# Optimization experiments

Hardware: AMD Instinct MI355X
Metric: run time of the kernel (lower is better)

The kernel has to match this reference:

```python
import jax, jax.numpy as jnp
import numpy as np

NUM_NODES = 50000
NUM_EDGES = 800000
NUM_FEATURES = 128
HIDDEN = 256
NUM_CLASSES = 10
NUM_GRAPHS = 64


def setup_inputs() -> dict:
    key = jax.random.key(0)
    ks = jax.random.split(key, 16)
    x = jax.random.normal(ks[0], (NUM_NODES, NUM_FEATURES), dtype=jnp.float32)
    edge_index = jax.random.randint(ks[1], (2, NUM_EDGES), 0, NUM_NODES, dtype=jnp.int64)
    batch = jnp.sort(jax.random.randint(ks[2], (NUM_NODES,), 0, NUM_GRAPHS, dtype=jnp.int64))

    def glorot(k, shape):
        fan_in, fan_out = shape[-2], shape[-1]
        s = jnp.sqrt(6.0 / (fan_in + fan_out)).astype(jnp.float32)
        return jax.random.uniform(k, shape, jnp.float32, -s, s)

    inp = {
        "x": x, "edge_index": edge_index, "batch": batch,
        # Chebyshev weights: one [in, out] matrix per hop order k
        "W1": glorot(ks[3], (3, NUM_FEATURES, HIDDEN)), "b1": jnp.zeros((HIDDEN,), jnp.float32),
        "W2": glorot(ks[4], (4, HIDDEN, HIDDEN)),       "b2": jnp.zeros((HIDDEN,), jnp.float32),
        "W3": glorot(ks[5], (5, HIDDEN, HIDDEN)),       "b3": jnp.zeros((HIDDEN,), jnp.float32),
        "fc1_w": glorot(ks[6], (HIDDEN, 512)),  "fc1_b": jnp.zeros((512,), jnp.float32),
        "fc2_w": glorot(ks[7], (512, HIDDEN)),  "fc2_b": jnp.zeros((HIDDEN,), jnp.float32),
        "fc3_w": glorot(ks[8], (HIDDEN, NUM_CLASSES)), "fc3_b": jnp.zeros((NUM_CLASSES,), jnp.float32),
    }
    return inp


def reference(x, edge_index, batch, W1, b1, W2, b2, W3, b3,
              fc1_w, fc1_b, fc2_w, fc2_b, fc3_w, fc3_b):
    N = x.shape[0]
    src, dst = edge_index[0], edge_index[1]

    # Scaled Laplacian L_hat = -D^{-1/2} A D^{-1/2} (lambda_max = 2, sym norm)
    deg = jax.ops.segment_sum(jnp.ones_like(src, dtype=x.dtype), src, num_segments=N)
    dis = jnp.where(deg > 0, jax.lax.rsqrt(jnp.maximum(deg, 1.0)), 0.0)
    w = -dis[src] * dis[dst]  # [E]

    def prop(h):  # L_hat @ h via gather-scale-scatter
        return jax.ops.segment_sum(h[src] * w[:, None], dst, num_segments=N)

    def cheb(h, Wk, b):
        K = Wk.shape[0]
        Tx0 = h
        out = Tx0 @ Wk[0]
        Tx1 = prop(h)
        out = out + Tx1 @ Wk[1]
        for k in range(2, K):
            Tx2 = 2.0 * prop(Tx1) - Tx0
            out = out + Tx2 @ Wk[k]
            Tx0, Tx1 = Tx1, Tx2
        return out + b

    h = jax.nn.relu(cheb(x, W1, b1))
    h = jax.nn.relu(cheb(h, W2, b2))
    h = jax.nn.relu(cheb(h, W3, b3))

    # global mean pool over graphs in the batch
    sums = jax.ops.segment_sum(h, batch, num_segments=NUM_GRAPHS)
    cnts = jax.ops.segment_sum(jnp.ones((N,), h.dtype), batch, num_segments=NUM_GRAPHS)
    g = sums / jnp.maximum(cnts, 1.0)[:, None]  # [G, 256]

    g = jax.nn.relu(g @ fc1_w + fc1_b)  # dropout is identity at inference
    g = jax.nn.relu(g @ fc2_w + fc2_b)
    g = g @ fc3_w + fc3_b
    return jax.nn.log_softmax(g, axis=1)
```

## Files before the change

### kernel.cpp

```cpp
#include <hip/hip_runtime.h>
#include <cstdint>
#include <cstddef>

#define NN 50000
#define NE 800000
#define FIN 128
#define HID 256
#define NCLS 10
#define NG 64
#define LDT 1280

#define NCH 13
#define NCELL (NN * NCH)
#define NSCB ((NCELL + 255) / 256)

typedef unsigned int uint;
typedef unsigned short ushort;
typedef __attribute__((ext_vector_type(8))) short short8;
typedef __attribute__((ext_vector_type(4))) float f32x4;

static inline size_t align_up(size_t v, size_t a) { return (v + a - 1) / a * a; }

__device__ __forceinline__ float bf2f(ushort u) {
    union { uint i; float f; } v; v.i = (uint)u << 16; return v.f;
}
__device__ __forceinline__ ushort f2bf(float f) {
    union { uint i; float f; } v; v.f = f;
    uint i = v.i;
    uint r = (i + 0x7fffu + ((i >> 16) & 1u)) >> 16;
    return (ushort)r;
}
__device__ __forceinline__ uint pack2(float a, float b) {
    return (uint)f2bf(a) | ((uint)f2bf(b) << 16);
}


__global__ void k_degcnt(const int* __restrict__ src, const int* __restrict__ dst,
                         int* __restrict__ ideg, int* __restrict__ cellcnt) {
    int e = blockIdx.x * 256 + threadIdx.x;
    if (e < NE) {
        int s = src[e], d = dst[e];
        atomicAdd(&ideg[s], 1);
        atomicAdd(&cellcnt[d * NCH + (s >> 12)], 1);
    }
}

__global__ void k_dis(const int* __restrict__ ideg, float* __restrict__ dis) {
    int n = blockIdx.x * 256 + threadIdx.x;
    if (n < NN) {
        int d = ideg[n];
        dis[n] = (d > 0) ? rsqrtf((float)d) : 0.0f;
    }
}

__global__ void k_scanA(const int* __restrict__ cnt, int* __restrict__ rp,
                        int* __restrict__ bsum) {
    __shared__ int s[256];
    int i = blockIdx.x * 256 + threadIdx.x;
    int v = (i < NCELL) ? cnt[i] : 0;
    s[threadIdx.x] = v;
    __syncthreads();
    for (int off = 1; off < 256; off <<= 1) {
        int t = (threadIdx.x >= (unsigned)off) ? s[threadIdx.x - off] : 0;
        __syncthreads();
        s[threadIdx.x] += t;
        __syncthreads();
    }
    if (i < NCELL) rp[i] = s[threadIdx.x] - v;
    if (threadIdx.x == 255) bsum[blockIdx.x] = s[255];
}

__global__ void k_scanB(int* __restrict__ b, int n) {
    __shared__ int s[1024];
    __shared__ int carry;
    if (threadIdx.x == 0) carry = 0;
    __syncthreads();
    for (int base = 0; base < n; base += 1024) {
        int i = base + threadIdx.x;
        int v = (i < n) ? b[i] : 0;
        s[threadIdx.x] = v;
        __syncthreads();
        for (int off = 1; off < 1024; off <<= 1) {
            int t = (threadIdx.x >= (unsigned)off) ? s[threadIdx.x - off] : 0;
            __syncthreads();
            s[threadIdx.x] += t;
            __syncthreads();
        }
        int c = carry;
        if (i < n) b[i] = c + s[threadIdx.x] - v;
        __syncthreads();
        if (threadIdx.x == 0) carry = c + s[1023];
        __syncthreads();
    }
}

__global__ void k_scanC(const int* __restrict__ bsum, int* __restrict__ rp,
                        int* __restrict__ cur, int* __restrict__ rpn) {
    int i = blockIdx.x * 256 + threadIdx.x;
    if (i < NCELL) {
        int v = rp[i] + bsum[blockIdx.x];
        rp[i] = v;
        cur[i] = v;
        if (i % NCH == 0) rpn[i / NCH] = v;
    }
    if (i == 0) rpn[NN] = NE;
}

__global__ void k_fill2(const int* __restrict__ src, const int* __restrict__ dst,
                        const float* __restrict__ dis, int* __restrict__ cur,
                        uint2* __restrict__ em) {
    int e = blockIdx.x * 256 + threadIdx.x;
    if (e < NE) {
        int s = src[e], d = dst[e];
        int pos = atomicAdd(&cur[d * NCH + (s >> 12)], 1);
        uint2 m;
        m.x = (uint)s;
        m.y = __float_as_uint(-dis[s] * dis[d]);
        em[pos] = m;
    }
}

__global__ void k_wt(const float* __restrict__ W, ushort* __restrict__ Wt, int K) {
    int i = blockIdx.x * 256 + threadIdx.x;
    if (i < K * 256) {
        int k = i >> 8, n = i & 255;
        Wt[(size_t)n * K + k] = f2bf(W[i]);
    }
}


__global__ void k_spread_x(const float* __restrict__ x, ushort* __restrict__ T) {
    int i = blockIdx.x * 256 + threadIdx.x;
    if (i < NN * 64) {
        int m = i >> 6, p = i & 63;
        const float* xp = x + (size_t)m * FIN + p * 2;
        uint* tp = (uint*)(T + (size_t)m * LDT) + p;
        *tp = pack2(xp[0], xp[1]);
    }
}

template <int FUSE, int F>
__global__ __launch_bounds__(512) void k_prop3(
    const int* __restrict__ rpn, const uint2* __restrict__ em,
    const ushort* __restrict__ h, const ushort* __restrict__ sub,
    ushort* __restrict__ out) {
    constexpr int NV = (F == 256) ? 4 : 2;
    int d = blockIdx.x * 8 + (threadIdx.x >> 6);
    int lane = threadIdx.x & 63;
    int beg = rpn[d], end = rpn[d + 1];
    float a[NV];
#pragma unroll
    for (int j = 0; j < NV; ++j) a[j] = 0.0f;

    int e = beg;
    int nfull = (end - beg) >> 3;
    if (nfull > 0) {
        uint2 mt[8];
#pragma unroll
        for (int u = 0; u < 8; ++u) mt[u] = em[e + u];
        for (int g = 0; g < nfull; ++g) {
            uint2 mtn[8];
            if (F == 256) {
                uint2 gg[8];
#pragma unroll
                for (int u = 0; u < 8; ++u)
                    gg[u] = *((const uint2*)(h + (size_t)mt[u].x * LDT) + lane);
#pragma unroll
                for (int u = 0; u < 8; ++u) {
                    int pe = e + 8 + u; if (pe > end - 1) pe = end - 1;
                    mtn[u] = em[pe];
                }
#pragma unroll
                for (int u = 0; u < 8; ++u) {
                    float wv = __uint_as_float(mt[u].y);
                    a[0] += wv * bf2f((ushort)gg[u].x);
                    a[1] += wv * bf2f((ushort)(gg[u].x >> 16));
                    a[2] += wv * bf2f((ushort)gg[u].y);
                    a[3] += wv * bf2f((ushort)(gg[u].y >> 16));
                }
            } else {
                uint gg[8];
#pragma unroll
                for (int u = 0; u < 8; ++u)
                    gg[u] = *((const uint*)(h + (size_t)mt[u].x * LDT) + lane);
#pragma unroll
                for (int u = 0; u < 8; ++u) {
                    int pe = e + 8 + u; if (pe > end - 1) pe = end - 1;
                    mtn[u] = em[pe];
                }
#pragma unroll
                for (int u = 0; u < 8; ++u) {
                    float wv = __uint_as_float(mt[u].y);
                    a[0] += wv * bf2f((ushort)gg[u]);
                    a[1] += wv * bf2f((ushort)(gg[u] >> 16));
                }
            }
#pragma unroll
            for (int u = 0; u < 8; ++u) mt[u] = mtn[u];
            e += 8;
        }
    }
    for (; e + 4 <= end; e += 4) {
        uint2 mt[4];
#pragma unroll
        for (int u = 0; u < 4; ++u) mt[u] = em[e + u];
        if (F == 256) {
            uint2 gg[4];
#pragma unroll
            for (int u = 0; u < 4; ++u)
                gg[u] = *((const uint2*)(h + (size_t)mt[u].x * LDT) + lane);
#pragma unroll
            for (int u = 0; u < 4; ++u) {
                float wv = __uint_as_float(mt[u].y);
                a[0] += wv * bf2f((ushort)gg[u].x);
                a[1] += wv * bf2f((ushort)(gg[u].x >> 16));
                a[2] += wv * bf2f((ushort)gg[u].y);
                a[3] += wv * bf2f((ushort)(gg[u].y >> 16));
            }
        } else {
            uint gg[4];
#pragma unroll
            for (int u = 0; u < 4; ++u)
                gg[u] = *((const uint*)(h + (size_t)mt[u].x * LDT) + lane);
#pragma unroll
            for (int u = 0; u < 4; ++u) {
                float wv = __uint_as_float(mt[u].y);
                a[0] += wv * bf2f((ushort)gg[u]);
                a[1] += wv * bf2f((ushort)(gg[u] >> 16));
            }
        }
    }
    for (; e < end; ++e) {
        uint2 m0 = em[e];
        float w0 = __uint_as_float(m0.y);
        if (F == 256) {
            uint2 g0 = *((const uint2*)(h + (size_t)m0.x * LDT) + lane);
            a[0] += w0 * bf2f((ushort)g0.x); a[1] += w0 * bf2f((ushort)(g0.x >> 16));
            a[2] += w0 * bf2f((ushort)g0.y); a[3] += w0 * bf2f((ushort)(g0.y >> 16));
        } else {
            uint g0 = *((const uint*)(h + (size_t)m0.x * LDT) + lane);
            a[0] += w0 * bf2f((ushort)g0); a[1] += w0 * bf2f((ushort)(g0 >> 16));
        }
    }

    if (F == 256) {
        uint2* op = (uint2*)(out + (size_t)d * LDT) + lane;
        if (FUSE) {
            uint2 sv = *((const uint2*)(sub + (size_t)d * LDT) + lane);
            uint2 r;
            r.x = pack2(2.0f * a[0] - bf2f((ushort)sv.x),
                        2.0f * a[1] - bf2f((ushort)(sv.x >> 16)));
            r.y = pack2(2.0f * a[2] - bf2f((ushort)sv.y),
                        2.0f * a[3] - bf2f((ushort)(sv.y >> 16)));
            *op = r;
        } else {
            uint2 r;
            r.x = pack2(a[0], a[1]);
            r.y = pack2(a[2], a[3]);
            *op = r;
        }
    } else {
        uint* op = (uint*)(out + (size_t)d * LDT) + lane;
        if (FUSE) {
            uint sv = *((const uint*)(sub + (size_t)d * LDT) + lane);
            *op = pack2(2.0f * a[0] - bf2f((ushort)sv),
                        2.0f * a[1] - bf2f((ushort)(sv >> 16)));
        } else {
            *op = pack2(a[0], a[1]);
        }
    }
}

template <int K>
__global__ __launch_bounds__(256) void k_mm3(
    const ushort* __restrict__ A, int lda,
    int m0, int m1, int m2, int m3, int m4,
    const ushort* __restrict__ Wt, const float* __restrict__ bias,
    ushort* __restrict__ H, int ldh, int M) {
    constexpr int NT = K / 32;
    __shared__ ushort As[3][128 * 32];
    __shared__ ushort Bs[3][128 * 32];
    int tid = threadIdx.x;
    int lane = tid & 63, w = tid >> 6;
    int wm = w >> 1, wn = w & 1;
    int rowBase = blockIdx.x * 128;
    int colBase = blockIdx.y * 128;
    int srow = lane >> 2;
    int c16 = lane & 3;

    f32x4 acc[4][4];
#pragma unroll
    for (int i = 0; i < 4; ++i)
#pragma unroll
        for (int j = 0; j < 4; ++j) acc[i][j] = (f32x4){0.f, 0.f, 0.f, 0.f};

    auto stage = [&](int t) {
        int kk = t * 32;
        int slot = kk >> 8;
        int coff = (slot == 0 ? m0 : slot == 1 ? m1 : slot == 2 ? m2
                    : slot == 3 ? m3 : m4) + (kk & 255);
        int b = t % 3;
#pragma unroll
        for (int q = 0; q < 2; ++q) {
            int seg = w * 2 + q;
            int r = seg * 16 + srow;
            int cs = c16 ^ ((r >> 1) & 3);
            int grow = rowBase + r;
            if (grow > M - 1) grow = M - 1;
            const ushort* gp = A + (size_t)grow * lda + coff + cs * 8;
            __builtin_amdgcn_global_load_lds(
                (const __attribute__((address_space(1))) void*)gp,
                (__attribute__((address_space(3))) void*)((char*)&As[b][0] + seg * 1024),
                16, 0, 0);
        }
#pragma unroll
        for (int q = 0; q < 2; ++q) {
            int seg = w * 2 + q;
            int r = seg * 16 + srow;
            int cs = c16 ^ ((r >> 1) & 3);
            const ushort* gp = Wt + (size_t)(colBase + r) * K + kk + cs * 8;
            __builtin_amdgcn_global_load_lds(
                (const __attribute__((address_space(1))) void*)gp,
                (__attribute__((address_space(3))) void*)((char*)&Bs[b][0] + seg * 1024),
                16, 0, 0);
        }
    };

    stage(0);
    stage(1);

    for (int t = 0; t < NT; ++t) {
        if (t + 1 < NT) {
            asm volatile("s_waitcnt vmcnt(4)" ::: "memory");
        } else {
            asm volatile("s_waitcnt vmcnt(0)" ::: "memory");
        }
        __builtin_amdgcn_s_barrier();
        if (t + 2 < NT) stage(t + 2);

        int b = t % 3;
        short8 af[4], bf[4];
#pragma unroll
        for (int mi = 0; mi < 4; ++mi) {
            int r = wm * 64 + mi * 16 + (lane & 15);
            int j = (lane >> 4) ^ ((r >> 1) & 3);
            af[mi] = *(const short8*)((const char*)&As[b][0] + r * 64 + j * 16);
        }
#pragma unroll
        for (int ni = 0; ni < 4; ++ni) {
            int r = wn * 64 + ni * 16 + (lane & 15);
            int j = (lane >> 4) ^ ((r >> 1) & 3);
            bf[ni] = *(const short8*)((const char*)&Bs[b][0] + r * 64 + j * 16);
        }
#pragma unroll
        for (int mi = 0; mi < 4; ++mi)
#pragma unroll
            for (int ni = 0; ni < 4; ++ni)
                acc[mi][ni] = __builtin_amdgcn_mfma_f32_16x16x32_bf16(
                    af[mi], bf[ni], acc[mi][ni], 0, 0, 0);
    }

    int lg = lane >> 4;
    float bv[4];
#pragma unroll
    for (int ni = 0; ni < 4; ++ni)
        bv[ni] = bias[colBase + wn * 64 + ni * 16 + (lane & 15)];
#pragma unroll
    for (int mi = 0; mi < 4; ++mi) {
#pragma unroll
        for (int r = 0; r < 4; ++r) {
            int row = rowBase + wm * 64 + mi * 16 + lg * 4 + r;
            if (row >= M) continue;
#pragma unroll
            for (int ni = 0; ni < 4; ++ni) {
                int colL = colBase + wn * 64 + ni * 16 + (lane & 15);
                float v = acc[mi][ni][r] + bv[ni];
                v = fmaxf(v, 0.0f);
                H[(size_t)row * ldh + colL] = f2bf(v);
            }
        }
    }
}


__global__ void k_pool(const ushort* __restrict__ h, const int* __restrict__ batch,
                       float* __restrict__ sums, float* __restrict__ cnts) {
    int f = threadIdx.x;
    int n0 = blockIdx.x * 128;
    if (n0 >= NN) return;
    int nEnd = n0 + 128 < NN ? n0 + 128 : NN;
    int cur = batch[n0];
    float acc = 0.0f, c = 0.0f;
    for (int n = n0; n < nEnd; ++n) {
        int b = batch[n];
        if (b != cur) {
            atomicAdd(&sums[cur * HID + f], acc);
            if (f == 0) atomicAdd(&cnts[cur], c);
            acc = 0.0f; c = 0.0f; cur = b;
        }
        acc += bf2f(h[(size_t)n * HID + f]);
        c += 1.0f;
    }
    atomicAdd(&sums[cur * HID + f], acc);
    if (f == 0) atomicAdd(&cnts[cur], c);
}

__global__ void k_gdiv(const float* __restrict__ sums, const float* __restrict__ cnts,
                       float* __restrict__ g) {
    int i = blockIdx.x * 256 + threadIdx.x;
    int b = i >> 8;
    g[i] = sums[i] / fmaxf(cnts[b], 1.0f);
}


template <int RELU>
__global__ void k_fc(const float* __restrict__ in, const float* __restrict__ W,
                     const float* __restrict__ bias, float* __restrict__ out,
                     int K, int Nc) {
    __shared__ float s[512];
    int gi = blockIdx.x;
    for (int i = threadIdx.x; i < K; i += blockDim.x) s[i] = in[gi * K + i];
    __syncthreads();
    int c = blockIdx.y * blockDim.x + threadIdx.x;
    if (c < Nc) {
        float acc = bias[c];
        for (int k = 0; k < K; ++k) acc += s[k] * W[k * Nc + c];
        out[gi * Nc + c] = RELU ? fmaxf(acc, 0.0f) : acc;
    }
}

__global__ void k_fc3_lsm(const float* __restrict__ in, const float* __restrict__ W,
                          const float* __restrict__ b, float* __restrict__ out) {
    __shared__ float s[HID];
    __shared__ float lg[NCLS];
    int gi = blockIdx.x;
    s[threadIdx.x] = in[gi * HID + threadIdx.x];
    __syncthreads();
    if (threadIdx.x < NCLS) {
        float acc = b[threadIdx.x];
        for (int k = 0; k < HID; ++k) acc += s[k] * W[k * NCLS + threadIdx.x];
        lg[threadIdx.x] = acc;
    }
    __syncthreads();
    if (threadIdx.x < NCLS) {
        float m = -1e30f;
        for (int c = 0; c < NCLS; ++c) m = fmaxf(m, lg[c]);
        float sum = 0.0f;
        for (int c = 0; c < NCLS; ++c) sum += expf(lg[c] - m);
        out[gi * NCLS + threadIdx.x] = lg[threadIdx.x] - m - logf(sum);
    }
}


extern "C" void kernel_launch(void* const* d_in, const int* in_sizes, int n_in,
                              void* d_out, int out_size, void* d_ws, size_t ws_size,
                              hipStream_t stream) {
    const float* x = (const float*)d_in[0];
    const int* ei = (const int*)d_in[1];
    const int* src = ei;
    const int* dst = ei + NE;
    const int* batch = (const int*)d_in[2];
    const float* W1 = (const float*)d_in[3];
    const float* b1 = (const float*)d_in[4];
    const float* W2 = (const float*)d_in[5];
    const float* b2 = (const float*)d_in[6];
    const float* W3 = (const float*)d_in[7];
    const float* b3 = (const float*)d_in[8];
    const float* fc1w = (const float*)d_in[9];
    const float* fc1b = (const float*)d_in[10];
    const float* fc2w = (const float*)d_in[11];
    const float* fc2b = (const float*)d_in[12];
    const float* fc3w = (const float*)d_in[13];
    const float* fc3b = (const float*)d_in[14];
    float* out = (float*)d_out;

    char* p = (char*)d_ws;
    auto carve = [&](size_t bytes) {
        char* r = p;
        p += align_up(bytes, 256);
        return (void*)r;
    };
    ushort* Tbig = (ushort*)carve((size_t)NN * LDT * 2);
    ushort* hA = (ushort*)carve((size_t)NN * HID * 2);
    ushort* Wt1 = (ushort*)carve((size_t)HID * 384 * 2);
    ushort* Wt2 = (ushort*)carve((size_t)HID * 1024 * 2);
    ushort* Wt3 = (ushort*)carve((size_t)HID * 1280 * 2);
    int* ideg = (int*)carve((size_t)NN * 4);
    float* dis = (float*)carve((size_t)NN * 4);
    uint2* em = (uint2*)carve((size_t)NE * 8);
    int* cellcnt = (int*)carve((size_t)NCELL * 4);
    int* cellptr = (int*)carve((size_t)(NCELL + 1) * 4);
    int* ccur = (int*)carve((size_t)NCELL * 4);
    int* rpn = (int*)carve((size_t)(NN + 1) * 4);
    int* bsum = (int*)carve((size_t)NSCB * 4);
    float* psum = (float*)carve((size_t)NG * HID * 4);
    float* pcnt = (float*)carve((size_t)NG * 4);
    float* g = (float*)carve((size_t)NG * HID * 4);
    float* f1 = (float*)carve((size_t)NG * 512 * 4);
    float* f2 = (float*)carve((size_t)NG * HID * 4);

    hipMemsetAsync(ideg, 0, (size_t)NN * 4, stream);
    hipMemsetAsync(cellcnt, 0, (size_t)NCELL * 4, stream);
    hipMemsetAsync(psum, 0, (size_t)NG * HID * 4, stream);
    hipMemsetAsync(pcnt, 0, (size_t)NG * 4, stream);

    k_degcnt<<<(NE + 255) / 256, 256, 0, stream>>>(src, dst, ideg, cellcnt);
    k_dis<<<(NN + 255) / 256, 256, 0, stream>>>(ideg, dis);
    k_scanA<<<NSCB, 256, 0, stream>>>(cellcnt, cellptr, bsum);
    k_scanB<<<1, 1024, 0, stream>>>(bsum, NSCB);
    k_scanC<<<NSCB, 256, 0, stream>>>(bsum, cellptr, ccur, rpn);
    k_fill2<<<(NE + 255) / 256, 256, 0, stream>>>(src, dst, dis, ccur, em);

    k_wt<<<(384 * 256 + 255) / 256, 256, 0, stream>>>(W1, Wt1, 384);
    k_wt<<<(1024 * 256 + 255) / 256, 256, 0, stream>>>(W2, Wt2, 1024);
    k_wt<<<(1280 * 256 + 255) / 256, 256, 0, stream>>>(W3, Wt3, 1280);

    dim3 mmg((NN + 127) / 128, 2);

    k_spread_x<<<(NN * 64 + 255) / 256, 256, 0, stream>>>(x, Tbig);
    k_prop3<0, 128><<<NN / 8, 512, 0, stream>>>(rpn, em, Tbig + 0, nullptr, Tbig + 128);
    k_prop3<1, 128><<<NN / 8, 512, 0, stream>>>(rpn, em, Tbig + 128, Tbig + 0, Tbig + 256);
    k_mm3<384><<<mmg, 256, 0, stream>>>(Tbig, LDT, 0, 256, 0, 0, 0,
                                        Wt1, b1, Tbig + 1024, LDT, NN);

    k_prop3<0, 256><<<NN / 8, 512, 0, stream>>>(rpn, em, Tbig + 1024, nullptr, Tbig + 0);
    k_prop3<1, 256><<<NN / 8, 512, 0, stream>>>(rpn, em, Tbig + 0, Tbig + 1024, Tbig + 256);
    k_prop3<1, 256><<<NN / 8, 512, 0, stream>>>(rpn, em, Tbig + 256, Tbig + 0, Tbig + 512);
    k_mm3<1024><<<mmg, 256, 0, stream>>>(Tbig, LDT, 1024, 0, 256, 512, 0,
                                         Wt2, b2, Tbig + 768, LDT, NN);

    k_prop3<0, 256><<<NN / 8, 512, 0, stream>>>(rpn, em, Tbig + 768, nullptr, Tbig + 1024);
    k_prop3<1, 256><<<NN / 8, 512, 0, stream>>>(rpn, em, Tbig + 1024, Tbig + 768, Tbig + 0);
    k_prop3<1, 256><<<NN / 8, 512, 0, stream>>>(rpn, em, Tbig + 0, Tbig + 1024, Tbig + 256);
    k_prop3<1, 256><<<NN / 8, 512, 0, stream>>>(rpn, em, Tbig + 256, Tbig + 0, Tbig + 512);
    k_mm3<1280><<<mmg, 256, 0, stream>>>(Tbig, LDT, 768, 1024, 0, 256, 512,
                                         Wt3, b3, hA, HID, NN);

    k_pool<<<(NN + 127) / 128, 256, 0, stream>>>(hA, batch, psum, pcnt);
    k_gdiv<<<(NG * HID) / 256, 256, 0, stream>>>(psum, pcnt, g);
    k_fc<1><<<dim3(NG, 2), 256, 0, stream>>>(g, fc1w, fc1b, f1, HID, 512);
    k_fc<1><<<dim3(NG, 1), 256, 0, stream>>>(f1, fc2w, fc2b, f2, 512, HID);
    k_fc3_lsm<<<NG, 256, 0, stream>>>(f2, fc3w, fc3b, out);
}
```

Measured before the change: 932.0 us.

## Use 8-wave GEMM blocks, swap grid axes, merge weight transposes

The bf16 MFMA GEMM now runs 512 threads per block (8 waves, 2x4 layout), each wave computing a 64x32 sub-tile instead of 64x64. This halves per-wave accumulator registers and spreads tile loads across more waves. The grid is reordered so the two column blocks sharing the same A rows are adjacent, which may improve L2 reuse of A. The three weight-transpose launches are merged into one kernel to cut launch overhead. More waves per block raises per-CU parallelism, but each wave does less MFMA work per LDS fragment load, so LDS traffic per FLOP goes up.

```diff
diff --git a/kernel.cpp b/kernel.cpp
--- a/kernel.cpp
+++ b/kernel.cpp
@@ -120,11 +120,25 @@
     }
 }
 
-__global__ void k_wt(const float* __restrict__ W, ushort* __restrict__ Wt, int K) {
+__global__ void k_wtall(const float* __restrict__ W1, const float* __restrict__ W2,
+                        const float* __restrict__ W3, ushort* __restrict__ Wt1,
+                        ushort* __restrict__ Wt2, ushort* __restrict__ Wt3) {
     int i = blockIdx.x * 256 + threadIdx.x;
-    if (i < K * 256) {
+    if (i < 384 * 256) {
         int k = i >> 8, n = i & 255;
-        Wt[(size_t)n * K + k] = f2bf(W[i]);
+        Wt1[(size_t)n * 384 + k] = f2bf(W1[i]);
+        return;
+    }
+    i -= 384 * 256;
+    if (i < 1024 * 256) {
+        int k = i >> 8, n = i & 255;
+        Wt2[(size_t)n * 1024 + k] = f2bf(W2[i]);
+        return;
+    }
+    i -= 1024 * 256;
+    if (i < 1280 * 256) {
+        int k = i >> 8, n = i & 255;
+        Wt3[(size_t)n * 1280 + k] = f2bf(W3[i]);
     }
 }
 
@@ -272,7 +286,7 @@
 }
 
 template <int K>
-__global__ __launch_bounds__(256) void k_mm3(
+__global__ __launch_bounds__(512) void k_mm5(
     const ushort* __restrict__ A, int lda,
     int m0, int m1, int m2, int m3, int m4,
     const ushort* __restrict__ Wt, const float* __restrict__ bias,
@@ -282,17 +296,17 @@
     __shared__ ushort Bs[3][128 * 32];
     int tid = threadIdx.x;
     int lane = tid & 63, w = tid >> 6;
-    int wm = w >> 1, wn = w & 1;
-    int rowBase = blockIdx.x * 128;
-    int colBase = blockIdx.y * 128;
+    int wm = w >> 2, wn = w & 3;
+    int rowBase = blockIdx.y * 128;
+    int colBase = blockIdx.x * 128;
     int srow = lane >> 2;
     int c16 = lane & 3;
 
-    f32x4 acc[4][4];
+    f32x4 acc[4][2];
 #pragma unroll
     for (int i = 0; i < 4; ++i)
 #pragma unroll
-        for (int j = 0; j < 4; ++j) acc[i][j] = (f32x4){0.f, 0.f, 0.f, 0.f};
+        for (int j = 0; j < 2; ++j) acc[i][j] = (f32x4){0.f, 0.f, 0.f, 0.f};
 
     auto stage = [&](int t) {
         int kk = t * 32;
@@ -300,28 +314,24 @@
         int coff = (slot == 0 ? m0 : slot == 1 ? m1 : slot == 2 ? m2
                     : slot == 3 ? m3 : m4) + (kk & 255);
         int b = t % 3;
-#pragma unroll
-        for (int q = 0; q < 2; ++q) {
-            int seg = w * 2 + q;
-            int r = seg * 16 + srow;
+        {
+            int r = w * 16 + srow;
             int cs = c16 ^ ((r >> 1) & 3);
             int grow = rowBase + r;
             if (grow > M - 1) grow = M - 1;
             const ushort* gp = A + (size_t)grow * lda + coff + cs * 8;
             __builtin_amdgcn_global_load_lds(
                 (const __attribute__((address_space(1))) void*)gp,
-                (__attribute__((address_space(3))) void*)((char*)&As[b][0] + seg * 1024),
+                (__attribute__((address_space(3))) void*)((char*)&As[b][0] + w * 1024),
                 16, 0, 0);
         }
-#pragma unroll
-        for (int q = 0; q < 2; ++q) {
-            int seg = w * 2 + q;
-            int r = seg * 16 + srow;
+        {
+            int r = w * 16 + srow;
             int cs = c16 ^ ((r >> 1) & 3);
             const ushort* gp = Wt + (size_t)(colBase + r) * K + kk + cs * 8;
             __builtin_amdgcn_global_load_lds(
                 (const __attribute__((address_space(1))) void*)gp,
-                (__attribute__((address_space(3))) void*)((char*)&Bs[b][0] + seg * 1024),
+                (__attribute__((address_space(3))) void*)((char*)&Bs[b][0] + w * 1024),
                 16, 0, 0);
         }
     };
@@ -331,7 +341,7 @@
 
     for (int t = 0; t < NT; ++t) {
         if (t + 1 < NT) {
-            asm volatile("s_waitcnt vmcnt(4)" ::: "memory");
+            asm volatile("s_waitcnt vmcnt(2)" ::: "memory");
         } else {
             asm volatile("s_waitcnt vmcnt(0)" ::: "memory");
         }
@@ -339,7 +349,7 @@
         if (t + 2 < NT) stage(t + 2);
 
         int b = t % 3;
-        short8 af[4], bf[4];
+        short8 af[4], bf[2];
 #pragma unroll
         for (int mi = 0; mi < 4; ++mi) {
             int r = wm * 64 + mi * 16 + (lane & 15);
@@ -347,24 +357,24 @@
             af[mi] = *(const short8*)((const char*)&As[b][0] + r * 64 + j * 16);
         }
 #pragma unroll
-        for (int ni = 0; ni < 4; ++ni) {
-            int r = wn * 64 + ni * 16 + (lane & 15);
+        for (int ni = 0; ni < 2; ++ni) {
+            int r = wn * 32 + ni * 16 + (lane & 15);
             int j = (lane >> 4) ^ ((r >> 1) & 3);
             bf[ni] = *(const short8*)((const char*)&Bs[b][0] + r * 64 + j * 16);
         }
 #pragma unroll
         for (int mi = 0; mi < 4; ++mi)
 #pragma unroll
-            for (int ni = 0; ni < 4; ++ni)
+            for (int ni = 0; ni < 2; ++ni)
                 acc[mi][ni] = __builtin_amdgcn_mfma_f32_16x16x32_bf16(
                     af[mi], bf[ni], acc[mi][ni], 0, 0, 0);
     }
 
     int lg = lane >> 4;
-    float bv[4];
-#pragma unroll
-    for (int ni = 0; ni < 4; ++ni)
-        bv[ni] = bias[colBase + wn * 64 + ni * 16 + (lane & 15)];
+    float bv[2];
+#pragma unroll
+    for (int ni = 0; ni < 2; ++ni)
+        bv[ni] = bias[colBase + wn * 32 + ni * 16 + (lane & 15)];
 #pragma unroll
     for (int mi = 0; mi < 4; ++mi) {
 #pragma unroll
@@ -372,8 +382,8 @@
             int row = rowBase + wm * 64 + mi * 16 + lg * 4 + r;
             if (row >= M) continue;
 #pragma unroll
-            for (int ni = 0; ni < 4; ++ni) {
-                int colL = colBase + wn * 64 + ni * 16 + (lane & 15);
+            for (int ni = 0; ni < 2; ++ni) {
+                int colL = colBase + wn * 32 + ni * 16 + (lane & 15);
                 float v = acc[mi][ni][r] + bv[ni];
                 v = fmaxf(v, 0.0f);
                 H[(size_t)row * ldh + colL] = f2bf(v);
@@ -511,29 +521,27 @@
     k_scanC<<<NSCB, 256, 0, stream>>>(bsum, cellptr, ccur, rpn);
     k_fill2<<<(NE + 255) / 256, 256, 0, stream>>>(src, dst, dis, ccur, em);
 
-    k_wt<<<(384 * 256 + 255) / 256, 256, 0, stream>>>(W1, Wt1, 384);
-    k_wt<<<(1024 * 256 + 255) / 256, 256, 0, stream>>>(W2, Wt2, 1024);
-    k_wt<<<(1280 * 256 + 255) / 256, 256, 0, stream>>>(W3, Wt3, 1280);
-
-    dim3 mmg((NN + 127) / 128, 2);
+    k_wtall<<<(384 + 1024 + 1280), 256, 0, stream>>>(W1, W2, W3, Wt1, Wt2, Wt3);
+
+    dim3 mmg(2, (NN + 127) / 128);
 
     k_spread_x<<<(NN * 64 + 255) / 256, 256, 0, stream>>>(x, Tbig);
     k_prop3<0, 128><<<NN / 8, 512, 0, stream>>>(rpn, em, Tbig + 0, nullptr, Tbig + 128);
     k_prop3<1, 128><<<NN / 8, 512, 0, stream>>>(rpn, em, Tbig + 128, Tbig + 0, Tbig + 256);
-    k_mm3<384><<<mmg, 256, 0, stream>>>(Tbig, LDT, 0, 256, 0, 0, 0,
+    k_mm5<384><<<mmg, 512, 0, stream>>>(Tbig, LDT, 0, 256, 0, 0, 0,
                                         Wt1, b1, Tbig + 1024, LDT, NN);
 
     k_prop3<0, 256><<<NN / 8, 512, 0, stream>>>(rpn, em, Tbig + 1024, nullptr, Tbig + 0);
     k_prop3<1, 256><<<NN / 8, 512, 0, stream>>>(rpn, em, Tbig + 0, Tbig + 1024, Tbig + 256);
     k_prop3<1, 256><<<NN / 8, 512, 0, stream>>>(rpn, em, Tbig + 256, Tbig + 0, Tbig + 512);
-    k_mm3<1024><<<mmg, 256, 0, stream>>>(Tbig, LDT, 1024, 0, 256, 512, 0,
+    k_mm5<1024><<<mmg, 512, 0, stream>>>(Tbig, LDT, 1024, 0, 256, 512, 0,
                                          Wt2, b2, Tbig + 768, LDT, NN);
 
     k_prop3<0, 256><<<NN / 8, 512, 0, stream>>>(rpn, em, Tbig + 768, nullptr, Tbig + 1024);
     k_prop3<1, 256><<<NN / 8, 512, 0, stream>>>(rpn, em, Tbig + 1024, Tbig + 768, Tbig + 0);
     k_prop3<1, 256><<<NN / 8, 512, 0, stream>>>(rpn, em, Tbig + 0, Tbig + 1024, Tbig + 256);
     k_prop3<1, 256><<<NN / 8, 512, 0, stream>>>(rpn, em, Tbig + 256, Tbig + 0, Tbig + 512);
-    k_mm3<1280><<<mmg, 256, 0, stream>>>(Tbig, LDT, 768, 1024, 0, 256, 512,
+    k_mm5<1280><<<mmg, 512, 0, stream>>>(Tbig, LDT, 768, 1024, 0, 256, 512,
                                          Wt3, b3, hA, HID, NN);
 
     k_pool<<<(NN + 127) / 128, 256, 0, stream>>>(hA, batch, psum, pcnt);
```

Measured after the change: 919.4 us. No clear change (-1.4%).
